# Kernel tuning notes

Hardware: AMD Instinct MI355X
Metric: run time of the kernel (lower is better)

Reference implementation:

```python
import jax, jax.numpy as jnp
import numpy as np

OUT_H, OUT_W = 7, 7          # pooled output size
SR = 2                        # sampling_ratio (samples per bin side)
SCALE = 0.25                  # spatial_scale (stride-4 FPN level)
EPS = 1e-8


def setup_inputs() -> dict:
    key = jax.random.key(0)
    k1, k2, k3, k4, k5, k6 = jax.random.split(key, 6)
    N, C, H, W = 2, 256, 200, 200
    R = 1000
    inp = jax.random.normal(k1, (N, C, H, W), dtype=jnp.float32)
    # rois: (batch_idx, x_ctr, y_ctr, width, height, angle_degrees) in image coords
    bidx = jax.random.randint(k2, (R,), 0, N).astype(jnp.float32)
    xc = jax.random.uniform(k3, (R,), minval=0.0, maxval=W / SCALE)
    yc = jax.random.uniform(k4, (R,), minval=0.0, maxval=H / SCALE)
    wh = jax.random.uniform(k5, (R, 2), minval=32.0, maxval=256.0)
    ang = jax.random.uniform(k6, (R,), minval=-90.0, maxval=90.0)
    rois = jnp.concatenate([bidx[:, None], xc[:, None], yc[:, None], wh, ang[:, None]], axis=1)
    return {"input": inp, "rois": rois}


def _roi_align_rotated(feat, rois):
    """Detectron2-style rotated RoIAlign (aligned, continuous coords).
    feat: [N,C,H,W] float; rois: [R,6] -> out [R,C,OUT_H,OUT_W]."""
    N, C, H, W = feat.shape
    R = rois.shape[0]
    b = rois[:, 0].astype(jnp.int32)
    cw = rois[:, 1] * SCALE - 0.5          # roi center (continuous pixel coords)
    ch = rois[:, 2] * SCALE - 0.5
    rw = jnp.maximum(rois[:, 3] * SCALE, 1.0)
    rh = jnp.maximum(rois[:, 4] * SCALE, 1.0)
    theta = rois[:, 5] * jnp.float32(np.pi / 180.0)
    cos_t, sin_t = jnp.cos(theta), jnp.sin(theta)

    bin_h = rh / OUT_H
    bin_w = rw / OUT_W
    # sample offsets within each bin: (i + 0.5)/SR for i in [0, SR)
    frac = (jnp.arange(SR, dtype=feat.dtype) + 0.5) / SR
    # local (un-rotated) coords relative to roi center: [R, OUT, SR]
    yy = (-rh / 2)[:, None, None] + (jnp.arange(OUT_H, dtype=feat.dtype)[None, :, None] + frac[None, None, :]) * bin_h[:, None, None]
    xx = (-rw / 2)[:, None, None] + (jnp.arange(OUT_W, dtype=feat.dtype)[None, :, None] + frac[None, None, :]) * bin_w[:, None, None]
    # rotate into feature-map coords: [R, PH, PW, GH, GW]
    yy5 = yy[:, :, None, :, None]
    xx5 = xx[:, None, :, None, :]
    c5 = cos_t[:, None, None, None, None]
    s5 = sin_t[:, None, None, None, None]
    y = yy5 * c5 - xx5 * s5 + ch[:, None, None, None, None]
    x = yy5 * s5 + xx5 * c5 + cw[:, None, None, None, None]

    S = OUT_H * OUT_W * SR * SR
    y = y.reshape(R, S)
    x = x.reshape(R, S)

    valid = (y >= -1.0) & (y <= H) & (x >= -1.0) & (x <= W)
    y = jnp.maximum(y, 0.0)
    x = jnp.maximum(x, 0.0)
    yl0 = jnp.floor(y).astype(jnp.int32)
    xl0 = jnp.floor(x).astype(jnp.int32)
    cy = yl0 >= H - 1
    cx = xl0 >= W - 1
    y_low = jnp.where(cy, H - 1, yl0)
    y_high = jnp.where(cy, H - 1, yl0 + 1)
    yv = jnp.where(cy, jnp.asarray(H - 1, feat.dtype), y)
    x_low = jnp.where(cx, W - 1, xl0)
    x_high = jnp.where(cx, W - 1, xl0 + 1)
    xv = jnp.where(cx, jnp.asarray(W - 1, feat.dtype), x)

    ly = yv - y_low.astype(feat.dtype)
    lx = xv - x_low.astype(feat.dtype)
    hy, hx = 1.0 - ly, 1.0 - lx
    w1, w2, w3, w4 = hy * hx, hy * lx, ly * hx, ly * lx

    bb = b[:, None]  # [R,1] broadcast against [R,S]
    v1 = feat[bb, :, y_low, x_low]    # [R,S,C]
    v2 = feat[bb, :, y_low, x_high]
    v3 = feat[bb, :, y_high, x_low]
    v4 = feat[bb, :, y_high, x_high]
    val = (w1[..., None] * v1 + w2[..., None] * v2
           + w3[..., None] * v3 + w4[..., None] * v4)
    val = jnp.where(valid[..., None], val, 0.0)
    # average over the SR*SR samples in each bin
    out = val.reshape(R, OUT_H, OUT_W, SR * SR, C).sum(axis=3) / (SR * SR)
    return out.transpose(0, 3, 1, 2)  # [R,C,PH,PW]


def reference(input, rois):
    out = _roi_align_rotated(input, rois)
    # wrapper applies torch.nan_to_num(roi_align, EPS, EPS, EPS)
    return jnp.nan_to_num(out, nan=EPS, posinf=EPS, neginf=EPS)
```

## Files before the change

### kernel.cpp

```cpp
#include <hip/hip_runtime.h>
#include <hip/hip_fp16.h>

#define FH 200
#define FW 200
#define FC 256
#define NBIN 49
#define NSAMP 196
#define OUTS_STRIDE 260

__device__ __forceinline__ void compute_sample(const float* __restrict__ roi,
                                               int s, bool nhwc,
                                               float4* wout, int4* oout)
{
    int   b  = (int)roi[0];
    float cw = roi[1] * 0.25f - 0.5f;
    float ch = roi[2] * 0.25f - 0.5f;
    float rw = fmaxf(roi[3] * 0.25f, 1.0f);
    float rh = fmaxf(roi[4] * 0.25f, 1.0f);
    float th = roi[5] * 0.017453292519943295f;
    float ct = cosf(th);
    float st = sinf(th);
    float bin_h = rh / 7.0f;
    float bin_w = rw / 7.0f;

    int bin = s >> 2;
    int sub = s & 3;
    int iy  = sub >> 1;
    int ix  = sub & 1;
    int ph  = bin / 7;
    int pw  = bin - ph * 7;

    float fy = 0.25f + 0.5f * (float)iy;
    float fx = 0.25f + 0.5f * (float)ix;
    float yy = -rh * 0.5f + ((float)ph + fy) * bin_h;
    float xx = -rw * 0.5f + ((float)pw + fx) * bin_w;
    float y  = yy * ct - xx * st + ch;
    float x  = yy * st + xx * ct + cw;

    bool valid = (y >= -1.0f) && (y <= (float)FH) && (x >= -1.0f) && (x <= (float)FW);
    y = fmaxf(y, 0.0f);
    x = fmaxf(x, 0.0f);
    int y0 = (int)floorf(y);
    int x0 = (int)floorf(x);
    bool cy = (y0 >= FH - 1);
    bool cx = (x0 >= FW - 1);
    int ylo = cy ? (FH - 1) : y0;
    int yhi = cy ? (FH - 1) : (y0 + 1);
    int xlo = cx ? (FW - 1) : x0;
    int xhi = cx ? (FW - 1) : (x0 + 1);
    float ly = cy ? 0.0f : (y - (float)y0);
    float lx = cx ? 0.0f : (x - (float)x0);
    float hy = 1.0f - ly;
    float hx = 1.0f - lx;
    float m  = valid ? 0.25f : 0.0f;

    *wout = make_float4(hy * hx * m, hy * lx * m, ly * hx * m, ly * lx * m);

    int bb = b * (FC * FH * FW);
    int p0 = ylo * FW + xlo;
    int p1 = ylo * FW + xhi;
    int p2 = yhi * FW + xlo;
    int p3 = yhi * FW + xhi;
    if (nhwc)
        *oout = make_int4(bb + p0 * FC, bb + p1 * FC, bb + p2 * FC, bb + p3 * FC);
    else
        *oout = make_int4(bb + p0, bb + p1, bb + p2, bb + p3);
}

__device__ __forceinline__ float fixnum(float v)
{
    return (v == v && v <= 3.402823466e38f && v >= -3.402823466e38f) ? v : 1e-8f;
}

__global__ __launch_bounds__(256)
void transpose_f16_kernel(const float* __restrict__ in, __half* __restrict__ out)
{
    __shared__ __half tileT[32][72];
    int b   = blockIdx.z;
    int p0  = blockIdx.x * 32;
    int c0  = blockIdx.y * 64;
    int tid = threadIdx.x;

    const float* inb  = in  + (size_t)b * FC * (FH * FW);
    __half*      outb = out + (size_t)b * (FH * FW) * FC;

#pragma unroll
    for (int k = 0; k < 2; ++k) {
        int chl = k * 32 + (tid >> 3);
        int px4 = (tid & 7) * 4;
        float4 v = *(const float4*)(inb + (size_t)(c0 + chl) * (FH * FW) + p0 + px4);
        tileT[px4 + 0][chl] = __float2half(v.x);
        tileT[px4 + 1][chl] = __float2half(v.y);
        tileT[px4 + 2][chl] = __float2half(v.z);
        tileT[px4 + 3][chl] = __float2half(v.w);
    }
    __syncthreads();

    int p  = tid >> 3;
    int h8 = (tid & 7) * 8;
    uint4 d = *(const uint4*)&tileT[p][h8];
    *(uint4*)(outb + (size_t)(p0 + p) * FC + c0 + h8) = d;
}

__global__ __launch_bounds__(256)
void roi_nhwc_f16_kernel(const __half* __restrict__ feat,
                         const float* __restrict__ rois,
                         float* __restrict__ out)
{
    __shared__ float4 s_w[NSAMP];
    __shared__ int4   s_o[NSAMP];
    __shared__ float  out_s[NBIN * OUTS_STRIDE];

    int r   = blockIdx.x;
    int tid = threadIdx.x;

    const float* roi = rois + r * 6;
    if (tid < NSAMP) {
        float4 w; int4 o;
        compute_sample(roi, tid, true, &w, &o);
        s_w[tid] = w;
        s_o[tid] = o;
    }
    __syncthreads();

    int w    = tid >> 6;
    int lane = tid & 63;
    int s2   = lane >> 5;
    int ch8  = (lane & 31) * 8;

    for (int p = w; p < 25; p += 4) {
        int bin = p * 2 + s2;
        if (bin < NBIN) {
            float acc[8];
#pragma unroll
            for (int i = 0; i < 8; ++i) acc[i] = 0.0f;

#pragma unroll
            for (int sub = 0; sub < 4; ++sub) {
                int s = bin * 4 + sub;
                float4 wt = s_w[s];
                int4   o  = s_o[s];
                uint4 u0 = *(const uint4*)(feat + o.x + ch8);
                uint4 u1 = *(const uint4*)(feat + o.y + ch8);
                uint4 u2 = *(const uint4*)(feat + o.z + ch8);
                uint4 u3 = *(const uint4*)(feat + o.w + ch8);
                const __half2* h0 = (const __half2*)&u0;
                const __half2* h1 = (const __half2*)&u1;
                const __half2* h2 = (const __half2*)&u2;
                const __half2* h3 = (const __half2*)&u3;
#pragma unroll
                for (int j = 0; j < 4; ++j) {
                    float2 f0 = __half22float2(h0[j]);
                    float2 f1 = __half22float2(h1[j]);
                    float2 f2 = __half22float2(h2[j]);
                    float2 f3 = __half22float2(h3[j]);
                    acc[2 * j + 0] += wt.x * f0.x + wt.y * f1.x + wt.z * f2.x + wt.w * f3.x;
                    acc[2 * j + 1] += wt.x * f0.y + wt.y * f1.y + wt.z * f2.y + wt.w * f3.y;
                }
            }
            float* dst = &out_s[bin * OUTS_STRIDE + ch8];
            *(float4*)(dst + 0) = make_float4(acc[0], acc[1], acc[2], acc[3]);
            *(float4*)(dst + 4) = make_float4(acc[4], acc[5], acc[6], acc[7]);
        }
    }
    __syncthreads();

    float* obase = out + (size_t)r * (FC * NBIN);
    for (int v4 = tid; v4 < (FC * NBIN) / 4; v4 += 256) {
        int f0 = v4 * 4;
        float vals[4];
#pragma unroll
        for (int i = 0; i < 4; ++i) {
            int f = f0 + i;
            int c = f / NBIN;
            int b = f - c * NBIN;
            vals[i] = fixnum(out_s[b * OUTS_STRIDE + c]);
        }
        *(float4*)(obase + f0) = make_float4(vals[0], vals[1], vals[2], vals[3]);
    }
}

__global__ __launch_bounds__(256)
void roi_nchw_kernel(const float* __restrict__ feat,
                     const float* __restrict__ rois,
                     float* __restrict__ out)
{
    int r   = blockIdx.x;
    int tid = threadIdx.x;

    __shared__ float4 s_w[NSAMP];
    __shared__ int4   s_o[NSAMP];

    const float* roi = rois + r * 6;
    if (tid < NSAMP) {
        float4 w; int4 o;
        compute_sample(roi, tid, false, &w, &o);
        s_w[tid] = w;
        s_o[tid] = o;
    }
    __syncthreads();

    const float* fc = feat + (size_t)tid * (FH * FW);
    float* obase = out + (size_t)r * (FC * NBIN) + (size_t)tid * NBIN;

    for (int bin = 0; bin < NBIN; ++bin) {
        float a = 0.0f;
#pragma unroll
        for (int k = 0; k < 4; ++k) {
            float4 w = s_w[bin * 4 + k];
            int4   o = s_o[bin * 4 + k];
            a += w.x * fc[o.x] + w.y * fc[o.y] + w.z * fc[o.z] + w.w * fc[o.w];
        }
        obase[bin] = fixnum(a);
    }
}

extern "C" void kernel_launch(void* const* d_in, const int* in_sizes, int n_in,
                              void* d_out, int out_size, void* d_ws, size_t ws_size,
                              hipStream_t stream)
{
    const float* feat = (const float*)d_in[0];
    const float* rois = (const float*)d_in[1];
    float* out = (float*)d_out;

    int R = in_sizes[1] / 6;
    int N = in_sizes[0] / (FC * FH * FW);
    size_t need = (size_t)in_sizes[0] * sizeof(__half);

    if (ws_size >= need) {
        __half* featT = (__half*)d_ws;
        dim3 tb(256, 1, 1);
        dim3 tg((FH * FW) / 32, FC / 64, N);
        transpose_f16_kernel<<<tg, tb, 0, stream>>>(feat, featT);
        roi_nhwc_f16_kernel<<<R, 256, 0, stream>>>(featT, rois, out);
    } else {
        roi_nchw_kernel<<<R, 256, 0, stream>>>(feat, rois, out);
    }
}
```

Baseline: 177.3 us.

## Split ROI kernel over channel halves with half-precision staging and swizzled transpose

The ROI kernel now launches two blocks per ROI, each handling 128 channels. Bins are spread across 16-thread groups, and results are staged in shared memory as fp16 instead of fp32, which shrinks LDS use and with launch bounds of 5 is meant to raise occupancy and parallelism. The transpose kernel gets an XOR swizzle to cut LDS bank conflicts. The cost is that per-sample weights and offsets are recomputed twice per ROI, and outputs are rounded to fp16 before being widened back to fp32, adding precision error.

```diff
diff --git a/kernel.cpp b/kernel.cpp
--- a/kernel.cpp
+++ b/kernel.cpp
@@ -3,10 +3,11 @@
 
 #define FH 200
 #define FW 200
+#define FHW 40000
 #define FC 256
 #define NBIN 49
 #define NSAMP 196
-#define OUTS_STRIDE 260
+#define OH_STRIDE 136
 
 __device__ __forceinline__ void compute_sample(const float* __restrict__ roi,
                                                int s, bool nhwc,
@@ -56,7 +57,7 @@
 
     *wout = make_float4(hy * hx * m, hy * lx * m, ly * hx * m, ly * lx * m);
 
-    int bb = b * (FC * FH * FW);
+    int bb = b * (FC * FHW);
     int p0 = ylo * FW + xlo;
     int p1 = ylo * FW + xhi;
     int p2 = yhi * FW + xlo;
@@ -75,43 +76,47 @@
 __global__ __launch_bounds__(256)
 void transpose_f16_kernel(const float* __restrict__ in, __half* __restrict__ out)
 {
-    __shared__ __half tileT[32][72];
+    __shared__ __align__(16) __half tileT[32][72];
     int b   = blockIdx.z;
     int p0  = blockIdx.x * 32;
     int c0  = blockIdx.y * 64;
     int tid = threadIdx.x;
 
-    const float* inb  = in  + (size_t)b * FC * (FH * FW);
-    __half*      outb = out + (size_t)b * (FH * FW) * FC;
+    const float* inb  = in  + (size_t)b * FC * FHW;
+    __half*      outb = out + (size_t)b * FHW * FC;
 
 #pragma unroll
     for (int k = 0; k < 2; ++k) {
         int chl = k * 32 + (tid >> 3);
         int px4 = (tid & 7) * 4;
-        float4 v = *(const float4*)(inb + (size_t)(c0 + chl) * (FH * FW) + p0 + px4);
-        tileT[px4 + 0][chl] = __float2half(v.x);
-        tileT[px4 + 1][chl] = __float2half(v.y);
-        tileT[px4 + 2][chl] = __float2half(v.z);
-        tileT[px4 + 3][chl] = __float2half(v.w);
-    }
-    __syncthreads();
-
-    int p  = tid >> 3;
-    int h8 = (tid & 7) * 8;
-    uint4 d = *(const uint4*)&tileT[p][h8];
-    *(uint4*)(outb + (size_t)(p0 + p) * FC + c0 + h8) = d;
-}
-
-__global__ __launch_bounds__(256)
+        float4 v = *(const float4*)(inb + (size_t)(c0 + chl) * FHW + p0 + px4);
+        int g   = ((chl >> 3) ^ (px4 >> 2)) & 7;
+        int col = (g << 3) | (chl & 7);
+        tileT[px4 + 0][col] = __float2half(v.x);
+        tileT[px4 + 1][col] = __float2half(v.y);
+        tileT[px4 + 2][col] = __float2half(v.z);
+        tileT[px4 + 3][col] = __float2half(v.w);
+    }
+    __syncthreads();
+
+    int p = tid >> 3;
+    int q = tid & 7;
+    int g = (q ^ ((p >> 2) & 7));
+    uint4 d = *(const uint4*)&tileT[p][g << 3];
+    *(uint4*)(outb + (size_t)(p0 + p) * FC + c0 + q * 8) = d;
+}
+
+__global__ __launch_bounds__(256, 5)
 void roi_nhwc_f16_kernel(const __half* __restrict__ feat,
                          const float* __restrict__ rois,
                          float* __restrict__ out)
 {
     __shared__ float4 s_w[NSAMP];
     __shared__ int4   s_o[NSAMP];
-    __shared__ float  out_s[NBIN * OUTS_STRIDE];
+    __shared__ __align__(16) __half out_h[NBIN * OH_STRIDE];
 
     int r   = blockIdx.x;
+    int c0  = blockIdx.y * 128;
     int tid = threadIdx.x;
 
     const float* roi = rois + r * 6;
@@ -123,50 +128,50 @@
     }
     __syncthreads();
 
-    int w    = tid >> 6;
-    int lane = tid & 63;
-    int s2   = lane >> 5;
-    int ch8  = (lane & 31) * 8;
-
-    for (int p = w; p < 25; p += 4) {
-        int bin = p * 2 + s2;
-        if (bin < NBIN) {
-            float acc[8];
-#pragma unroll
-            for (int i = 0; i < 8; ++i) acc[i] = 0.0f;
-
-#pragma unroll
-            for (int sub = 0; sub < 4; ++sub) {
-                int s = bin * 4 + sub;
-                float4 wt = s_w[s];
-                int4   o  = s_o[s];
-                uint4 u0 = *(const uint4*)(feat + o.x + ch8);
-                uint4 u1 = *(const uint4*)(feat + o.y + ch8);
-                uint4 u2 = *(const uint4*)(feat + o.z + ch8);
-                uint4 u3 = *(const uint4*)(feat + o.w + ch8);
-                const __half2* h0 = (const __half2*)&u0;
-                const __half2* h1 = (const __half2*)&u1;
-                const __half2* h2 = (const __half2*)&u2;
-                const __half2* h3 = (const __half2*)&u3;
-#pragma unroll
-                for (int j = 0; j < 4; ++j) {
-                    float2 f0 = __half22float2(h0[j]);
-                    float2 f1 = __half22float2(h1[j]);
-                    float2 f2 = __half22float2(h2[j]);
-                    float2 f3 = __half22float2(h3[j]);
-                    acc[2 * j + 0] += wt.x * f0.x + wt.y * f1.x + wt.z * f2.x + wt.w * f3.x;
-                    acc[2 * j + 1] += wt.x * f0.y + wt.y * f1.y + wt.z * f2.y + wt.w * f3.y;
-                }
+    int grp    = tid >> 4;
+    int lane16 = tid & 15;
+    int ch8    = lane16 * 8;
+
+    const __half* fbase = feat + c0 + ch8;
+
+    for (int bin = grp; bin < NBIN; bin += 16) {
+        float acc[8];
+#pragma unroll
+        for (int i = 0; i < 8; ++i) acc[i] = 0.0f;
+
+#pragma unroll
+        for (int sub = 0; sub < 4; ++sub) {
+            int s = bin * 4 + sub;
+            float4 wt = s_w[s];
+            int4   o  = s_o[s];
+            uint4 u0 = *(const uint4*)(fbase + o.x);
+            uint4 u1 = *(const uint4*)(fbase + o.y);
+            uint4 u2 = *(const uint4*)(fbase + o.z);
+            uint4 u3 = *(const uint4*)(fbase + o.w);
+            const __half2* h0 = (const __half2*)&u0;
+            const __half2* h1 = (const __half2*)&u1;
+            const __half2* h2 = (const __half2*)&u2;
+            const __half2* h3 = (const __half2*)&u3;
+#pragma unroll
+            for (int j = 0; j < 4; ++j) {
+                float2 f0 = __half22float2(h0[j]);
+                float2 f1 = __half22float2(h1[j]);
+                float2 f2 = __half22float2(h2[j]);
+                float2 f3 = __half22float2(h3[j]);
+                acc[2 * j + 0] += wt.x * f0.x + wt.y * f1.x + wt.z * f2.x + wt.w * f3.x;
+                acc[2 * j + 1] += wt.x * f0.y + wt.y * f1.y + wt.z * f2.y + wt.w * f3.y;
             }
-            float* dst = &out_s[bin * OUTS_STRIDE + ch8];
-            *(float4*)(dst + 0) = make_float4(acc[0], acc[1], acc[2], acc[3]);
-            *(float4*)(dst + 4) = make_float4(acc[4], acc[5], acc[6], acc[7]);
         }
-    }
-    __syncthreads();
-
-    float* obase = out + (size_t)r * (FC * NBIN);
-    for (int v4 = tid; v4 < (FC * NBIN) / 4; v4 += 256) {
+        __half2 hv[4];
+#pragma unroll
+        for (int j = 0; j < 4; ++j)
+            hv[j] = __floats2half2_rn(acc[2 * j + 0], acc[2 * j + 1]);
+        *(uint4*)&out_h[bin * OH_STRIDE + ch8] = *(const uint4*)hv;
+    }
+    __syncthreads();
+
+    float* obase = out + (size_t)r * (FC * NBIN) + (size_t)blockIdx.y * (128 * NBIN);
+    for (int v4 = tid; v4 < (128 * NBIN) / 4; v4 += 256) {
         int f0 = v4 * 4;
         float vals[4];
 #pragma unroll
@@ -174,7 +179,7 @@
             int f = f0 + i;
             int c = f / NBIN;
             int b = f - c * NBIN;
-            vals[i] = fixnum(out_s[b * OUTS_STRIDE + c]);
+            vals[i] = fixnum(__half2float(out_h[b * OH_STRIDE + c]));
         }
         *(float4*)(obase + f0) = make_float4(vals[0], vals[1], vals[2], vals[3]);
     }
@@ -200,7 +205,7 @@
     }
     __syncthreads();
 
-    const float* fc = feat + (size_t)tid * (FH * FW);
+    const float* fc = feat + (size_t)tid * FHW;
     float* obase = out + (size_t)r * (FC * NBIN) + (size_t)tid * NBIN;
 
     for (int bin = 0; bin < NBIN; ++bin) {
@@ -224,15 +229,15 @@
     float* out = (float*)d_out;
 
     int R = in_sizes[1] / 6;
-    int N = in_sizes[0] / (FC * FH * FW);
+    int N = in_sizes[0] / (FC * FHW);
     size_t need = (size_t)in_sizes[0] * sizeof(__half);
 
     if (ws_size >= need) {
         __half* featT = (__half*)d_ws;
-        dim3 tb(256, 1, 1);
-        dim3 tg((FH * FW) / 32, FC / 64, N);
-        transpose_f16_kernel<<<tg, tb, 0, stream>>>(feat, featT);
-        roi_nhwc_f16_kernel<<<R, 256, 0, stream>>>(featT, rois, out);
+        dim3 tg(FHW / 32, FC / 64, N);
+        transpose_f16_kernel<<<tg, 256, 0, stream>>>(feat, featT);
+        dim3 g(R, 2, 1);
+        roi_nhwc_f16_kernel<<<g, 256, 0, stream>>>(featT, rois, out);
     } else {
         roi_nchw_kernel<<<R, 256, 0, stream>>>(feat, rois, out);
     }
```

New measurement: 272.5 us. 1.54x slower.
